# Optimization experiments

Measured on AMD Instinct MI355X. Metric: run time of the kernel, lower is better.

## Reference

```python
import jax, jax.numpy as jnp
import numpy as np

B, V, H = 4, 256, 128
BN_EPS = 1e-5


def setup_inputs() -> dict:
    key = jax.random.key(0)
    ks = jax.random.split(key, 20)
    n = lambda k, shape, s=1.0: jax.random.normal(k, shape, dtype=jnp.float32) * s
    return {
        "h": n(ks[0], (B, V, H)),
        "e": n(ks[1], (B, V, V, H)),
        "x": jax.random.uniform(ks[2], (B, V, 2), dtype=jnp.float32),
        "graph": jax.random.randint(ks[3], (B, V, V), 0, 2, dtype=jnp.int32),
        "Uw": n(ks[4], (H, H), 0.05), "Ub": n(ks[5], (H,), 0.05),
        "Vw": n(ks[6], (H, H), 0.05), "Vb": n(ks[7], (H,), 0.05),
        "Aw": n(ks[8], (H, H), 0.05), "Ab": n(ks[9], (H,), 0.05),
        "Bw": n(ks[10], (H, H), 0.05), "Bb": n(ks[11], (H,), 0.05),
        "Cw": n(ks[12], (H, H), 0.05), "Cb": n(ks[13], (H,), 0.05),
        "dw": n(ks[14], (H, 1), 0.05), "db": n(ks[15], (H,), 0.05),
        "ew": n(ks[16], (1, H), 0.05), "eb": n(ks[17], (1,), 0.05),
        "c": n(ks[18], (1,), 0.1),
        "gamma_h": jnp.ones((H,), jnp.float32), "beta_h": jnp.zeros((H,), jnp.float32),
        "gamma_e": jnp.ones((H,), jnp.float32), "beta_e": jnp.zeros((H,), jnp.float32),
    }


def _batchnorm(z, gamma, beta):
    # BatchNorm1d over flattened leading dims (batch statistics, biased var)
    zf = z.reshape(-1, z.shape[-1])
    mu = zf.mean(0)
    var = zf.var(0)
    return (z - mu) * jax.lax.rsqrt(var + BN_EPS) * gamma + beta


def reference(h, e, x, graph, Uw, Ub, Vw, Vb, Aw, Ab, Bw, Bb, Cw, Cb,
              dw, db, ew, eb, c, gamma_h, beta_h, gamma_e, beta_e):
    lin = lambda z, W, b: jnp.einsum('...i,oi->...o', z, W) + b
    Uh = lin(h, Uw, Ub)                      # B V H
    Vh = lin(h, Vw, Vb)                      # B V H (node-j features)
    Ah = lin(h, Aw, Ab)
    Bh = lin(h, Bw, Bb)
    Ce = lin(e, Cw, Cb)                      # B V V H

    # diff[b,i,j] = x_i - x_j  (== x_to - x_from in the torch code)
    diff = x[:, :, None, :] - x[:, None, :, :]          # B V V 2
    d2 = jnp.sum(diff * diff, axis=-1, keepdims=True)   # B V V 1
    dist = jnp.where(d2 > 0, jnp.sqrt(jnp.where(d2 > 0, d2, 1.0)), 0.0)

    # e_ij = Ah_j + Bh_i + Ce_ij + d(|x_i - x_j|)
    e_new = Ah[:, None, :, :] + Bh[:, :, None, :] + Ce + dist * dw[:, 0] + db
    gates = jax.nn.sigmoid(e_new)                        # B V V H
    pa = jax.nn.sigmoid(jnp.einsum('bijh,oh->bijo', e_new, ew) + eb)  # B V V 1

    x_upd = c * jnp.sum(pa * diff, axis=2)               # B V 2

    # aggregate: zero out where graph == 1 (disconnected), sum over j
    msg = jnp.where(graph[..., None] == 1, 0.0, gates * Vh[:, None, :, :])
    h_new = Uh + jnp.sum(msg, axis=2)                    # B V H

    h_new = jax.nn.relu(_batchnorm(h_new, gamma_h, beta_h))
    e_out = jax.nn.relu(_batchnorm(e_new, gamma_e, beta_e))

    return (h + h_new, e + e_out, x + x_upd)
```

## Files before the change

### kernel.cpp

```cpp
#include <hip/hip_runtime.h>
#include <math.h>

#define BB 4
#define VV 256
#define HH 128
#define NBI (BB*VV)
#define NE  (NBI*VV)
#define BN_EPS 1e-5f

typedef short  short8  __attribute__((ext_vector_type(8)));
typedef float  floatx4 __attribute__((ext_vector_type(4)));

__device__ __forceinline__ float sigmoidf_(float v) {
    return 1.0f / (1.0f + __expf(-v));
}

__device__ __forceinline__ unsigned f2bf(float f) {
    union { float f; unsigned u; } c; c.f = f;
    unsigned u = c.u;
    return (u + 0x7fffu + ((u >> 16) & 1u)) >> 16;
}

__global__ __launch_bounds__(128)
void k1_lin4(const float* __restrict__ h,
             const float* __restrict__ Uw, const float* __restrict__ Ub,
             const float* __restrict__ Vw, const float* __restrict__ Vb,
             const float* __restrict__ Aw, const float* __restrict__ Ab,
             const float* __restrict__ Bw, const float* __restrict__ Bb,
             const float* __restrict__ Cw,
             float* __restrict__ Uh, float* __restrict__ Vh,
             float* __restrict__ Ah, float* __restrict__ Bh,
             unsigned short* __restrict__ cwp)
{
    __shared__ float sh[HH];
    int bi = blockIdx.x;
    int o  = threadIdx.x;

    if (bi < 128) {
        int idx  = bi*128 + o;
        int j    = idx & 7;
        int slot = idx >> 3;
        int lane = slot & 63;
        int tile = slot >> 6;
        int ht   = tile & 7;
        int ks   = tile >> 3;
        int k    = ks*32 + (lane >> 4)*8 + j;
        int hh   = ht*16 + (lane & 15);
        cwp[idx] = (unsigned short)f2bf(Cw[hh*HH + k]);
    }

    sh[o] = h[bi*HH + o];
    __syncthreads();

    float su = Ub[o], sv = Vb[o], sa = Ab[o], sb = Bb[o];
    const float4* sh4 = (const float4*)sh;
    const float4* Uw4 = (const float4*)Uw;
    const float4* Vw4 = (const float4*)Vw;
    const float4* Aw4 = (const float4*)Aw;
    const float4* Bw4 = (const float4*)Bw;
    #pragma unroll 8
    for (int k4 = 0; k4 < 32; ++k4) {
        float4 hv = sh4[k4];
        float4 wu = Uw4[o*32 + k4];
        float4 wv = Vw4[o*32 + k4];
        float4 wa = Aw4[o*32 + k4];
        float4 wb = Bw4[o*32 + k4];
        su += hv.x*wu.x + hv.y*wu.y + hv.z*wu.z + hv.w*wu.w;
        sv += hv.x*wv.x + hv.y*wv.y + hv.z*wv.z + hv.w*wv.w;
        sa += hv.x*wa.x + hv.y*wa.y + hv.z*wa.z + hv.w*wa.w;
        sb += hv.x*wb.x + hv.y*wb.y + hv.z*wb.z + hv.w*wb.w;
    }
    Uh[bi*HH + o] = su;
    Vh[bi*HH + o] = sv;
    Ah[bi*HH + o] = sa;
    Bh[bi*HH + o] = sb;
}

__global__ __launch_bounds__(256, 2)
void k2_main(const float* __restrict__ e,
             const float* __restrict__ x,
             const int*   __restrict__ graph,
             const unsigned short* __restrict__ cwp,
             const float* __restrict__ Cb,
             const float* __restrict__ dw, const float* __restrict__ db,
             const float* __restrict__ ew, const float* __restrict__ ebp,
             const float* __restrict__ Uh, const float* __restrict__ Vh,
             const float* __restrict__ Ah, const float* __restrict__ Bh,
             float* __restrict__ e_new,
             float* __restrict__ epart,
             float* __restrict__ hacc,
             float* __restrict__ xupd)
{
    __shared__ unsigned short s_b[16384];
    __shared__ float s_dist[128], s_dx[128], s_dy[128];
    __shared__ int   s_g[128];
    __shared__ float s_red[4*HH];

    int tid  = threadIdx.x;
    int bi   = blockIdx.x;
    int b    = bi >> 8;
    int lane = tid & 63;
    int w    = tid >> 6;
    int hl   = lane & 15;
    int q    = lane >> 4;

    {
        const int4* src = (const int4*)cwp;
        int4* dst = (int4*)s_b;
        #pragma unroll
        for (int it = 0; it < 8; ++it) dst[tid + it*256] = src[tid + it*256];
    }

    float pre[8], dwv[8], ewv[8];
    #pragma unroll
    for (int ht = 0; ht < 8; ++ht) {
        int hh = ht*16 + hl;
        pre[ht] = Bh[bi*HH + hh] + Cb[hh] + db[hh];
        dwv[ht] = dw[hh];
        ewv[ht] = ew[hh];
    }
    float ebv = ebp[0];
    float xi0 = x[bi*2 + 0], xi1 = x[bi*2 + 1];

    float ssum[8] = {0,0,0,0,0,0,0,0};
    float ssq [8] = {0,0,0,0,0,0,0,0};
    float hsum[8] = {0,0,0,0,0,0,0,0};
    float xa0 = 0.f, xa1 = 0.f;

    for (int chunk = 0; chunk < 2; ++chunk) {
        __syncthreads();
        if (tid < 128) {
            int j = chunk*128 + tid;
            float xj0 = x[(b*VV + j)*2 + 0], xj1 = x[(b*VV + j)*2 + 1];
            float dx = xi0 - xj0, dy = xi1 - xj1;
            float d2 = dx*dx + dy*dy;
            s_dx[tid] = dx; s_dy[tid] = dy;
            s_dist[tid] = (d2 > 0.f) ? sqrtf(d2) : 0.f;
            s_g[tid] = graph[(size_t)bi*VV + j];
        }
        __syncthreads();

        floatx4 acc[2][8];
        #pragma unroll
        for (int jt = 0; jt < 2; ++jt)
            #pragma unroll
            for (int ht = 0; ht < 8; ++ht)
                acc[jt][ht] = (floatx4){0.f,0.f,0.f,0.f};

        int j0 = chunk*128 + w*32;
        const float* eA0 = e + ((size_t)bi*VV + j0 + hl)*HH;
        const float* eA1 = eA0 + 16*HH;
        int koff = q*8;

        #pragma unroll
        for (int ks = 0; ks < 4; ++ks) {
            union { short8 s8; unsigned u[4]; } a0, a1;
            {
                const float* p = eA0 + ks*32 + koff;
                float4 u0 = *(const float4*)p;
                float4 u1 = *(const float4*)(p + 4);
                a0.u[0] = f2bf(u0.x) | (f2bf(u0.y) << 16);
                a0.u[1] = f2bf(u0.z) | (f2bf(u0.w) << 16);
                a0.u[2] = f2bf(u1.x) | (f2bf(u1.y) << 16);
                a0.u[3] = f2bf(u1.z) | (f2bf(u1.w) << 16);
            }
            {
                const float* p = eA1 + ks*32 + koff;
                float4 u0 = *(const float4*)p;
                float4 u1 = *(const float4*)(p + 4);
                a1.u[0] = f2bf(u0.x) | (f2bf(u0.y) << 16);
                a1.u[1] = f2bf(u0.z) | (f2bf(u0.w) << 16);
                a1.u[2] = f2bf(u1.x) | (f2bf(u1.y) << 16);
                a1.u[3] = f2bf(u1.z) | (f2bf(u1.w) << 16);
            }
            #pragma unroll
            for (int ht = 0; ht < 8; ++ht) {
                short8 bf = *(const short8*)(s_b + ((size_t)((ks*8 + ht)*64 + lane))*8);
                acc[0][ht] = __builtin_amdgcn_mfma_f32_16x16x32_bf16(a0.s8, bf, acc[0][ht], 0, 0, 0);
                acc[1][ht] = __builtin_amdgcn_mfma_f32_16x16x32_bf16(a1.s8, bf, acc[1][ht], 0, 0, 0);
            }
        }

        #pragma unroll
        for (int jt = 0; jt < 2; ++jt) {
            #pragma unroll
            for (int reg = 0; reg < 4; ++reg) {
                int jl = w*32 + jt*16 + q*4 + reg;
                int j  = chunk*128 + jl;
                float dist = s_dist[jl], dx = s_dx[jl], dy = s_dy[jl];
                int g = s_g[jl];
                const float* ahp = Ah + ((size_t)(b*VV + j))*HH;
                const float* vhp = Vh + ((size_t)(b*VV + j))*HH;
                float* enp = e_new + ((size_t)bi*VV + j)*HH;
                float padot = 0.f;
                #pragma unroll
                for (int ht = 0; ht < 8; ++ht) {
                    int hh = ht*16 + hl;
                    float en = acc[jt][ht][reg] + ahp[hh] + pre[ht] + dist*dwv[ht];
                    enp[hh] = en;
                    ssum[ht] += en;
                    ssq[ht]  += en*en;
                    padot    += en*ewv[ht];
                    if (g != 1) hsum[ht] += sigmoidf_(en) * vhp[hh];
                }
                padot += __shfl_xor(padot, 1);
                padot += __shfl_xor(padot, 2);
                padot += __shfl_xor(padot, 4);
                padot += __shfl_xor(padot, 8);
                if (hl == 0) {
                    float pa = sigmoidf_(padot + ebv);
                    xa0 += pa * dx;
                    xa1 += pa * dy;
                }
            }
        }
    }

    #pragma unroll
    for (int ht = 0; ht < 8; ++ht) {
        ssum[ht] += __shfl_xor(ssum[ht], 16); ssum[ht] += __shfl_xor(ssum[ht], 32);
        ssq[ht]  += __shfl_xor(ssq[ht],  16); ssq[ht]  += __shfl_xor(ssq[ht],  32);
        hsum[ht] += __shfl_xor(hsum[ht], 16); hsum[ht] += __shfl_xor(hsum[ht], 32);
    }

    __syncthreads();
    if (lane < 16) {
        #pragma unroll
        for (int ht = 0; ht < 8; ++ht) s_red[w*HH + ht*16 + lane] = ssum[ht];
    }
    __syncthreads();
    if (tid < HH)
        epart[(size_t)bi*2*HH + tid] =
            s_red[tid] + s_red[HH + tid] + s_red[2*HH + tid] + s_red[3*HH + tid];
    __syncthreads();
    if (lane < 16) {
        #pragma unroll
        for (int ht = 0; ht < 8; ++ht) s_red[w*HH + ht*16 + lane] = ssq[ht];
    }
    __syncthreads();
    if (tid < HH)
        epart[(size_t)bi*2*HH + HH + tid] =
            s_red[tid] + s_red[HH + tid] + s_red[2*HH + tid] + s_red[3*HH + tid];
    __syncthreads();
    if (lane < 16) {
        #pragma unroll
        for (int ht = 0; ht < 8; ++ht) s_red[w*HH + ht*16 + lane] = hsum[ht];
    }
    __syncthreads();
    if (tid < HH)
        hacc[bi*HH + tid] = Uh[bi*HH + tid] +
            s_red[tid] + s_red[HH + tid] + s_red[2*HH + tid] + s_red[3*HH + tid];
    __syncthreads();
    if (hl == 0) { s_red[w*4 + q] = xa0; s_red[16 + w*4 + q] = xa1; }
    __syncthreads();
    if (tid == 0) {
        float sx = 0.f, sy = 0.f;
        #pragma unroll
        for (int t = 0; t < 16; ++t) { sx += s_red[t]; sy += s_red[16 + t]; }
        xupd[bi*2 + 0] = sx;
        xupd[bi*2 + 1] = sy;
    }
}

__global__ __launch_bounds__(256)
void k3_stats(const float* __restrict__ epart, const float* __restrict__ hacc,
              const float* __restrict__ gamma_e, const float* __restrict__ beta_e,
              const float* __restrict__ gamma_h, const float* __restrict__ beta_h,
              float* __restrict__ coefs)
{
    __shared__ float rs[256], rq[256];
    int c = blockIdx.x, tid = threadIdx.x;
    float s = 0, q = 0;
    if (c < HH) {
        for (int r = tid; r < NBI; r += 256) {
            s += epart[(size_t)r*2*HH + c];
            q += epart[(size_t)r*2*HH + HH + c];
        }
    } else {
        int hh = c - HH;
        for (int r = tid; r < NBI; r += 256) {
            float v = hacc[r*HH + hh];
            s += v; q += v*v;
        }
    }
    rs[tid] = s; rq[tid] = q;
    __syncthreads();
    for (int off = 128; off > 0; off >>= 1) {
        if (tid < off) { rs[tid] += rs[tid+off]; rq[tid] += rq[tid+off]; }
        __syncthreads();
    }
    if (tid == 0) {
        float n = (c < HH) ? (float)NE : (float)NBI;
        float mean = rs[0] / n;
        float var  = rq[0] / n - mean*mean;
        int hh; float g, be;
        if (c < HH) { hh = c;      g = gamma_e[hh]; be = beta_e[hh]; }
        else        { hh = c - HH; g = gamma_h[hh]; be = beta_h[hh]; }
        float scale = g * rsqrtf(var + BN_EPS);
        float shift = be - mean*scale;
        if (c < HH) { coefs[hh]        = scale; coefs[HH + hh]   = shift; }
        else        { coefs[2*HH + hh] = scale; coefs[3*HH + hh] = shift; }
    }
}

__global__ __launch_bounds__(256)
void k4_eout(const float* __restrict__ e, const float* __restrict__ coefs,
             const float* __restrict__ h, const float* __restrict__ x,
             const float* __restrict__ hacc, const float* __restrict__ xupd,
             const float* __restrict__ cp,
             float* __restrict__ out0, float* __restrict__ out2,
             float* __restrict__ out1)
{
    int gid = blockIdx.x*256 + threadIdx.x;
    if (gid < NBI*HH) {
        int hh = gid & 127;
        float v = hacc[gid]*coefs[2*HH + hh] + coefs[3*HH + hh];
        out0[gid] = h[gid] + fmaxf(v, 0.f);
        if (gid < NBI*2) out2[gid] = x[gid] + cp[0]*xupd[gid];
    }

    const float4* e4 = (const float4*)e;
    float4* o4 = (float4*)out1;
    const float4* sc4 = (const float4*)coefs;
    const float4* sh4 = (const float4*)(coefs + HH);
    const int total = NE * (HH/4);
    for (int i = gid; i < total; i += gridDim.x*256) {
        int hq = i & 31;
        float4 en = o4[i];
        float4 ev = e4[i];
        float4 sc = sc4[hq], sh = sh4[hq];
        float4 r;
        r.x = ev.x + fmaxf(en.x*sc.x + sh.x, 0.f);
        r.y = ev.y + fmaxf(en.y*sc.y + sh.y, 0.f);
        r.z = ev.z + fmaxf(en.z*sc.z + sh.z, 0.f);
        r.w = ev.w + fmaxf(en.w*sc.w + sh.w, 0.f);
        o4[i] = r;
    }
}

extern "C" void kernel_launch(void* const* d_in, const int* in_sizes, int n_in,
                              void* d_out, int out_size, void* d_ws, size_t ws_size,
                              hipStream_t stream)
{
    (void)in_sizes; (void)n_in; (void)out_size; (void)ws_size;
    const float* h     = (const float*)d_in[0];
    const float* e     = (const float*)d_in[1];
    const float* x     = (const float*)d_in[2];
    const int*   graph = (const int*)d_in[3];
    const float* Uw = (const float*)d_in[4];
    const float* Ub = (const float*)d_in[5];
    const float* Vw = (const float*)d_in[6];
    const float* Vb = (const float*)d_in[7];
    const float* Aw = (const float*)d_in[8];
    const float* Ab = (const float*)d_in[9];
    const float* Bw = (const float*)d_in[10];
    const float* Bbv = (const float*)d_in[11];
    const float* Cw = (const float*)d_in[12];
    const float* Cb = (const float*)d_in[13];
    const float* dw = (const float*)d_in[14];
    const float* db = (const float*)d_in[15];
    const float* ew = (const float*)d_in[16];
    const float* eb = (const float*)d_in[17];
    const float* c  = (const float*)d_in[18];
    const float* gamma_h = (const float*)d_in[19];
    const float* beta_h  = (const float*)d_in[20];
    const float* gamma_e = (const float*)d_in[21];
    const float* beta_e  = (const float*)d_in[22];

    float* out0 = (float*)d_out;
    float* out1 = out0 + NBI*HH;
    float* out2 = out1 + (size_t)NE*HH;

    float* ws    = (float*)d_ws;
    float* Uh    = ws;
    float* Vh    = Uh + NBI*HH;
    float* Ah    = Vh + NBI*HH;
    float* Bh    = Ah + NBI*HH;
    float* hacc  = Bh + NBI*HH;
    float* epart = hacc + NBI*HH;
    float* xupd  = epart + (size_t)NBI*2*HH;
    float* coefs = xupd + NBI*2;
    unsigned short* cwp = (unsigned short*)(coefs + 4*HH);

    k1_lin4<<<NBI, 128, 0, stream>>>(h, Uw, Ub, Vw, Vb, Aw, Ab, Bw, Bbv, Cw,
                                     Uh, Vh, Ah, Bh, cwp);
    k2_main<<<NBI, 256, 0, stream>>>(e, x, graph, cwp, Cb, dw, db, ew, eb,
                                     Uh, Vh, Ah, Bh, out1, epart, hacc, xupd);
    k3_stats<<<2*HH, 256, 0, stream>>>(epart, hacc, gamma_e, beta_e,
                                       gamma_h, beta_h, coefs);
    k4_eout<<<4096, 256, 0, stream>>>(e, coefs, h, x, hacc, xupd, c,
                                      out0, out2, out1);
}
```

Baseline: 465.9 us.

## Stash e_new as fp16 and switch MFMA to f16 with higher occupancy

```diff
diff --git a/kernel.cpp b/kernel.cpp
--- a/kernel.cpp
+++ b/kernel.cpp
@@ -8,17 +8,21 @@
 #define NE  (NBI*VV)
 #define BN_EPS 1e-5f
 
-typedef short  short8  __attribute__((ext_vector_type(8)));
-typedef float  floatx4 __attribute__((ext_vector_type(4)));
+typedef _Float16 half8_ __attribute__((ext_vector_type(8)));
+typedef float    floatx4 __attribute__((ext_vector_type(4)));
 
 __device__ __forceinline__ float sigmoidf_(float v) {
     return 1.0f / (1.0f + __expf(-v));
 }
 
-__device__ __forceinline__ unsigned f2bf(float f) {
-    union { float f; unsigned u; } c; c.f = f;
-    unsigned u = c.u;
-    return (u + 0x7fffu + ((u >> 16) & 1u)) >> 16;
+__device__ __forceinline__ unsigned pk(float x, float y) {
+    auto h = __builtin_amdgcn_cvt_pkrtz(x, y);
+    return __builtin_bit_cast(unsigned, h);
+}
+
+__device__ __forceinline__ float h2f(unsigned short u) {
+    _Float16 h = __builtin_bit_cast(_Float16, u);
+    return (float)h;
 }
 
 __global__ __launch_bounds__(128)
@@ -46,7 +50,8 @@
         int ks   = tile >> 3;
         int k    = ks*32 + (lane >> 4)*8 + j;
         int hh   = ht*16 + (lane & 15);
-        cwp[idx] = (unsigned short)f2bf(Cw[hh*HH + k]);
+        _Float16 hv = (_Float16)Cw[hh*HH + k];
+        cwp[idx] = __builtin_bit_cast(unsigned short, hv);
     }
 
     sh[o] = h[bi*HH + o];
@@ -76,7 +81,7 @@
     Bh[bi*HH + o] = sb;
 }
 
-__global__ __launch_bounds__(256, 2)
+__global__ __launch_bounds__(256, 4)
 void k2_main(const float* __restrict__ e,
              const float* __restrict__ x,
              const int*   __restrict__ graph,
@@ -86,14 +91,14 @@
              const float* __restrict__ ew, const float* __restrict__ ebp,
              const float* __restrict__ Uh, const float* __restrict__ Vh,
              const float* __restrict__ Ah, const float* __restrict__ Bh,
-             float* __restrict__ e_new,
+             uint4* __restrict__ stash,
              float* __restrict__ epart,
              float* __restrict__ hacc,
              float* __restrict__ xupd)
 {
     __shared__ unsigned short s_b[16384];
-    __shared__ float s_dist[128], s_dx[128], s_dy[128];
-    __shared__ int   s_g[128];
+    __shared__ float s_dist[256], s_dx[256], s_dy[256];
+    __shared__ int   s_g[256];
     __shared__ float s_red[4*HH];
 
     int tid  = threadIdx.x;
@@ -111,6 +116,17 @@
         for (int it = 0; it < 8; ++it) dst[tid + it*256] = src[tid + it*256];
     }
 
+    float xi0 = x[bi*2 + 0], xi1 = x[bi*2 + 1];
+    {
+        int j = tid;
+        float xj0 = x[(b*VV + j)*2 + 0], xj1 = x[(b*VV + j)*2 + 1];
+        float dx = xi0 - xj0, dy = xi1 - xj1;
+        float d2 = dx*dx + dy*dy;
+        s_dx[j] = dx; s_dy[j] = dy;
+        s_dist[j] = (d2 > 0.f) ? sqrtf(d2) : 0.f;
+        s_g[j] = graph[(size_t)bi*VV + j];
+    }
+
     float pre[8], dwv[8], ewv[8];
     #pragma unroll
     for (int ht = 0; ht < 8; ++ht) {
@@ -120,98 +136,89 @@
         ewv[ht] = ew[hh];
     }
     float ebv = ebp[0];
-    float xi0 = x[bi*2 + 0], xi1 = x[bi*2 + 1];
+
+    __syncthreads();
 
     float ssum[8] = {0,0,0,0,0,0,0,0};
     float ssq [8] = {0,0,0,0,0,0,0,0};
     float hsum[8] = {0,0,0,0,0,0,0,0};
     float xa0 = 0.f, xa1 = 0.f;
 
-    for (int chunk = 0; chunk < 2; ++chunk) {
-        __syncthreads();
-        if (tid < 128) {
-            int j = chunk*128 + tid;
-            float xj0 = x[(b*VV + j)*2 + 0], xj1 = x[(b*VV + j)*2 + 1];
-            float dx = xi0 - xj0, dy = xi1 - xj1;
-            float d2 = dx*dx + dy*dy;
-            s_dx[tid] = dx; s_dy[tid] = dy;
-            s_dist[tid] = (d2 > 0.f) ? sqrtf(d2) : 0.f;
-            s_g[tid] = graph[(size_t)bi*VV + j];
+    #pragma unroll
+    for (int ch = 0; ch < 4; ++ch) {
+        int chunk = ch >> 1, half = ch & 1;
+        int j0 = chunk*128 + w*32 + half*16;
+        const float* eA = e + ((size_t)bi*VV + j0 + hl)*HH + q*8;
+
+        float4 L[8];
+        #pragma unroll
+        for (int ks = 0; ks < 4; ++ks) {
+            L[2*ks]   = *(const float4*)(eA + ks*32);
+            L[2*ks+1] = *(const float4*)(eA + ks*32 + 4);
         }
-        __syncthreads();
-
-        floatx4 acc[2][8];
-        #pragma unroll
-        for (int jt = 0; jt < 2; ++jt)
-            #pragma unroll
-            for (int ht = 0; ht < 8; ++ht)
-                acc[jt][ht] = (floatx4){0.f,0.f,0.f,0.f};
-
-        int j0 = chunk*128 + w*32;
-        const float* eA0 = e + ((size_t)bi*VV + j0 + hl)*HH;
-        const float* eA1 = eA0 + 16*HH;
-        int koff = q*8;
+
+        floatx4 acc[8];
+        #pragma unroll
+        for (int ht = 0; ht < 8; ++ht) acc[ht] = (floatx4){0.f,0.f,0.f,0.f};
 
         #pragma unroll
         for (int ks = 0; ks < 4; ++ks) {
-            union { short8 s8; unsigned u[4]; } a0, a1;
-            {
-                const float* p = eA0 + ks*32 + koff;
-                float4 u0 = *(const float4*)p;
-                float4 u1 = *(const float4*)(p + 4);
-                a0.u[0] = f2bf(u0.x) | (f2bf(u0.y) << 16);
-                a0.u[1] = f2bf(u0.z) | (f2bf(u0.w) << 16);
-                a0.u[2] = f2bf(u1.x) | (f2bf(u1.y) << 16);
-                a0.u[3] = f2bf(u1.z) | (f2bf(u1.w) << 16);
-            }
-            {
-                const float* p = eA1 + ks*32 + koff;
-                float4 u0 = *(const float4*)p;
-                float4 u1 = *(const float4*)(p + 4);
-                a1.u[0] = f2bf(u0.x) | (f2bf(u0.y) << 16);
-                a1.u[1] = f2bf(u0.z) | (f2bf(u0.w) << 16);
-                a1.u[2] = f2bf(u1.x) | (f2bf(u1.y) << 16);
-                a1.u[3] = f2bf(u1.z) | (f2bf(u1.w) << 16);
-            }
+            union { half8_ h; unsigned u[4]; } a;
+            a.u[0] = pk(L[2*ks].x,   L[2*ks].y);
+            a.u[1] = pk(L[2*ks].z,   L[2*ks].w);
+            a.u[2] = pk(L[2*ks+1].x, L[2*ks+1].y);
+            a.u[3] = pk(L[2*ks+1].z, L[2*ks+1].w);
             #pragma unroll
             for (int ht = 0; ht < 8; ++ht) {
-                short8 bf = *(const short8*)(s_b + ((size_t)((ks*8 + ht)*64 + lane))*8);
-                acc[0][ht] = __builtin_amdgcn_mfma_f32_16x16x32_bf16(a0.s8, bf, acc[0][ht], 0, 0, 0);
-                acc[1][ht] = __builtin_amdgcn_mfma_f32_16x16x32_bf16(a1.s8, bf, acc[1][ht], 0, 0, 0);
+                half8_ bf = *(const half8_*)(s_b + ((size_t)((ks*8 + ht)*64 + lane))*8);
+                acc[ht] = __builtin_amdgcn_mfma_f32_16x16x32_f16(a.h, bf, acc[ht], 0, 0, 0);
             }
         }
 
-        #pragma unroll
-        for (int jt = 0; jt < 2; ++jt) {
+        int jb = j0 + q*4;
+        #pragma unroll
+        for (int u = 0; u < 4; ++u) {
+            int j = jb + u;
+            const float* ap = Ah + ((size_t)(b*VV) + j)*HH + hl;
+            const float* vp = Vh + ((size_t)(b*VV) + j)*HH + hl;
+            float Av[8], Vv[8];
             #pragma unroll
-            for (int reg = 0; reg < 4; ++reg) {
-                int jl = w*32 + jt*16 + q*4 + reg;
-                int j  = chunk*128 + jl;
-                float dist = s_dist[jl], dx = s_dx[jl], dy = s_dy[jl];
-                int g = s_g[jl];
-                const float* ahp = Ah + ((size_t)(b*VV + j))*HH;
-                const float* vhp = Vh + ((size_t)(b*VV + j))*HH;
-                float* enp = e_new + ((size_t)bi*VV + j)*HH;
-                float padot = 0.f;
+            for (int ht = 0; ht < 8; ++ht) { Av[ht] = ap[ht*16]; Vv[ht] = vp[ht*16]; }
+
+            float dist = s_dist[j], dx = s_dx[j], dy = s_dy[j];
+            int g = s_g[j];
+
+            float en[8];
+            float padot = 0.f;
+            #pragma unroll
+            for (int ht = 0; ht < 8; ++ht) {
+                float v = acc[ht][u] + Av[ht] + pre[ht] + dist*dwv[ht];
+                en[ht] = v;
+                ssum[ht] += v;
+                ssq[ht]  += v*v;
+                padot    += v*ewv[ht];
+            }
+            if (g != 1) {
                 #pragma unroll
-                for (int ht = 0; ht < 8; ++ht) {
-                    int hh = ht*16 + hl;
-                    float en = acc[jt][ht][reg] + ahp[hh] + pre[ht] + dist*dwv[ht];
-                    enp[hh] = en;
-                    ssum[ht] += en;
-                    ssq[ht]  += en*en;
-                    padot    += en*ewv[ht];
-                    if (g != 1) hsum[ht] += sigmoidf_(en) * vhp[hh];
-                }
-                padot += __shfl_xor(padot, 1);
-                padot += __shfl_xor(padot, 2);
-                padot += __shfl_xor(padot, 4);
-                padot += __shfl_xor(padot, 8);
-                if (hl == 0) {
-                    float pa = sigmoidf_(padot + ebv);
-                    xa0 += pa * dx;
-                    xa1 += pa * dy;
-                }
+                for (int ht = 0; ht < 8; ++ht)
+                    hsum[ht] += sigmoidf_(en[ht]) * Vv[ht];
+            }
+
+            uint4 st;
+            st.x = pk(en[0], en[1]);
+            st.y = pk(en[2], en[3]);
+            st.z = pk(en[4], en[5]);
+            st.w = pk(en[6], en[7]);
+            stash[((size_t)bi*VV + j)*32 + hl] = st;
+
+            padot += __shfl_xor(padot, 1);
+            padot += __shfl_xor(padot, 2);
+            padot += __shfl_xor(padot, 4);
+            padot += __shfl_xor(padot, 8);
+            if (hl == 0) {
+                float pa = sigmoidf_(padot + ebv);
+                xa0 += pa * dx;
+                xa1 += pa * dy;
             }
         }
     }
@@ -311,7 +318,9 @@
              float* __restrict__ out0, float* __restrict__ out2,
              float* __restrict__ out1)
 {
-    int gid = blockIdx.x*256 + threadIdx.x;
+    __shared__ unsigned short s_t[64*144];
+    int tid = threadIdx.x;
+    int gid = blockIdx.x*256 + tid;
     if (gid < NBI*HH) {
         int hh = gid & 127;
         float v = hacc[gid]*coefs[2*HH + hh] + coefs[3*HH + hh];
@@ -319,22 +328,42 @@
         if (gid < NBI*2) out2[gid] = x[gid] + cp[0]*xupd[gid];
     }
 
-    const float4* e4 = (const float4*)e;
-    float4* o4 = (float4*)out1;
+    size_t r0 = (size_t)blockIdx.x * 64;
+    const uint4* sp = (const uint4*)out1;
+    #pragma unroll
+    for (int it = 0; it < 4; ++it) {
+        int rr = it*16 + (tid >> 4);
+        int sg = tid & 15;
+        *(uint4*)(s_t + rr*144 + sg*8) = sp[(r0 + rr)*32 + sg];
+    }
+    __syncthreads();
+
+    const float4* e4  = (const float4*)e;
+    float4* o4        = (float4*)out1;
     const float4* sc4 = (const float4*)coefs;
     const float4* sh4 = (const float4*)(coefs + HH);
-    const int total = NE * (HH/4);
-    for (int i = gid; i < total; i += gridDim.x*256) {
-        int hq = i & 31;
-        float4 en = o4[i];
-        float4 ev = e4[i];
-        float4 sc = sc4[hq], sh = sh4[hq];
-        float4 r;
-        r.x = ev.x + fmaxf(en.x*sc.x + sh.x, 0.f);
-        r.y = ev.y + fmaxf(en.y*sc.y + sh.y, 0.f);
-        r.z = ev.z + fmaxf(en.z*sc.z + sh.z, 0.f);
-        r.w = ev.w + fmaxf(en.w*sc.w + sh.w, 0.f);
-        o4[i] = r;
+    #pragma unroll
+    for (int k = 0; k < 8; ++k) {
+        int f  = k*256 + tid;
+        int r  = f >> 5;
+        int c4 = f & 31;
+        size_t gi = (r0 + r)*32 + c4;
+        float4 ev = e4[gi];
+        float4 sc = sc4[c4], sh = sh4[c4];
+        const unsigned short* row = s_t + r*144;
+        int cc = c4*4;
+        int pb = (cc & 15)*8 + (cc >> 4);
+        float4 en;
+        en.x = h2f(row[pb]);
+        en.y = h2f(row[pb + 8]);
+        en.z = h2f(row[pb + 16]);
+        en.w = h2f(row[pb + 24]);
+        float4 rr;
+        rr.x = ev.x + fmaxf(en.x*sc.x + sh.x, 0.f);
+        rr.y = ev.y + fmaxf(en.y*sc.y + sh.y, 0.f);
+        rr.z = ev.z + fmaxf(en.z*sc.z + sh.z, 0.f);
+        rr.w = ev.w + fmaxf(en.w*sc.w + sh.w, 0.f);
+        o4[gi] = rr;
     }
 }
 
@@ -385,9 +414,10 @@
     k1_lin4<<<NBI, 128, 0, stream>>>(h, Uw, Ub, Vw, Vb, Aw, Ab, Bw, Bbv, Cw,
                                      Uh, Vh, Ah, Bh, cwp);
     k2_main<<<NBI, 256, 0, stream>>>(e, x, graph, cwp, Cb, dw, db, ew, eb,
-                                     Uh, Vh, Ah, Bh, out1, epart, hacc, xupd);
+                                     Uh, Vh, Ah, Bh, (uint4*)out1,
+                                     epart, hacc, xupd);
     k3_stats<<<2*HH, 256, 0, stream>>>(epart, hacc, gamma_e, beta_e,
                                        gamma_h, beta_h, coefs);
-    k4_eout<<<4096, 256, 0, stream>>>(e, coefs, h, x, hacc, xupd, c,
-                                      out0, out2, out1);
-}
+    k4_eout<<<NE/64, 256, 0, stream>>>(e, coefs, h, x, hacc, xupd, c,
+                                       out0, out2, out1);
+}
```

After: 459.4 us. No clear change (-1.4%).
